# Kernel tuning notes

Hardware: AMD Instinct MI355X
Metric: run time of the kernel (lower is better)

## Reference

```python
import jax, jax.numpy as jnp
import numpy as np

SHIFT_PX = 2
SHIFT_TEMP = 0.07


def _normalize(x):
    # F.normalize(dim=-1): x / max(||x||, eps)
    n = jnp.linalg.norm(x, axis=-1, keepdims=True)
    return x / jnp.maximum(n, 1e-12)


def _weights_to_tokens(w):
    # w: [B,1,H,W] already at target_hw -> bilinear resize is identity
    wf = w.reshape(w.shape[0], -1)
    return wf / (wf.sum(axis=1, keepdims=True) + 1e-10)


def setup_inputs() -> dict:
    key = jax.random.key(0)
    k1, k2, k3, k4 = jax.random.split(key, 4)
    B, H, W, D = 8, 96, 96, 768
    N = H * W
    return {
        "z1": jax.random.normal(k1, (B, N, D), dtype=jnp.float32),
        "z2": jax.random.normal(k2, (B, N, D), dtype=jnp.float32),
        "w1": jax.random.uniform(k3, (B, 1, H, W), dtype=jnp.float32),
        "w2": jax.random.uniform(k4, (B, 1, H, W), dtype=jnp.float32),
        "H": H,
        "W": W,
    }


def reference(z1, z2, w1, w2, H, W):
    B, N, D = z1.shape
    # gs1 == gs2 == target_hw -> token interpolation is the identity shortcut
    z1g = _normalize(z1).reshape(B, H, W, D)
    z2g = _normalize(z2).reshape(B, H, W, D)

    w_avg = 0.5 * (_weights_to_tokens(w1) + _weights_to_tokens(w2))  # [B, N]

    r = SHIFT_PX
    # zero-pad so shifted reads outside the grid contribute zero similarity,
    # matching torch F.pad + slice semantics in the original loop
    z2pad = jnp.pad(z2g, ((0, 0), (r, r), (r, r), (0, 0)))
    sims = []
    for dy in range(-r, r + 1):
        for dx in range(-r, r + 1):
            # z2p[y, x] = z2g[y - dy, x - dx] (zeros out of range)
            z2p = z2pad[:, r - dy:r - dy + H, r - dx:r - dx + W, :]
            sims.append(jnp.einsum('bhwd,bhwd->bhw', z1g, z2p))
    sim_stack = jnp.stack(sims, axis=1)  # [B, (2r+1)^2, H, W]

    alpha = jax.nn.softmax(sim_stack / (SHIFT_TEMP + 1e-10), axis=1)
    sim_softbest = (alpha * sim_stack).sum(axis=1).reshape(B, -1)  # [B, N]

    align_loss = ((1.0 - sim_softbest) * w_avg).sum(axis=1).mean()
    pos_similarity = sim_softbest.mean()
    return jnp.stack([align_loss, pos_similarity])
```

## Files before the change

kernel.cpp:

```cpp
#include <hip/hip_runtime.h>
#include <hip/hip_bf16.h>

#define Bb 8
#define Hh 96
#define Ww 96
#define Dd 768
#define Nn (Hh*Ww)
#define DC 16
#define NCH (Dd/DC)
#define SZ 20
#define TMP 0.07f


__global__ __launch_bounds__(256) void k_wsum(const float* __restrict__ w1,
                                              const float* __restrict__ w2,
                                              float* __restrict__ ws) {
    int j = blockIdx.x;
    const float* src = (j < 8 ? w1 : w2) + (size_t)(j & 7) * Nn;
    float s = 0.f;
    for (int i = threadIdx.x; i < Nn; i += 256) s += src[i];
    for (int off = 32; off > 0; off >>= 1) s += __shfl_down(s, off, 64);
    __shared__ float parts[4];
    int lane = threadIdx.x & 63, wv = threadIdx.x >> 6;
    if (lane == 0) parts[wv] = s;
    __syncthreads();
    if (threadIdx.x == 0) ws[2 + j] = parts[0] + parts[1] + parts[2] + parts[3];
    if (j == 0 && threadIdx.x == 64) ws[0] = 0.f;
    if (j == 0 && threadIdx.x == 65) ws[1] = 0.f;
}

__global__ __launch_bounds__(384, 1) void k_main(
    const float* __restrict__ z1, const float* __restrict__ z2,
    const float* __restrict__ w1, const float* __restrict__ w2,
    float* __restrict__ ws) {
    extern __shared__ float sm[];
    float* z1s  = sm;
    float* z2s  = z1s + 96*SZ;
    float* simS = z2s + 5*100*SZ;
    float* nrm1 = simS + 25*96;
    float* nrm2 = nrm1 + 96;
    float* red  = nrm2 + 480;

    const int t = threadIdx.x;
    const int b = blockIdx.x / Hh;
    const int h = blockIdx.x % Hh;
    const int w = t % 96;
    const int quarter = t / 96;
    const int dq = quarter * 4;

    for (int i = t; i < 5*100*SZ; i += 384) z2s[i] = 0.f;
    for (int i = t; i < 25*96 + 96 + 480 + 2; i += 384) simS[i] = 0.f;

    float acc[5][5] = {};
    float nz2[5]    = {};
    float nz1       = 0.f;

    const size_t zbase = (size_t)b * Nn * Dd;

    for (int c = 0; c < NCH; ++c) {
        const int d0 = c * DC;
        __syncthreads();
        {
            int tok = t >> 2, j = t & 3;
            float4 v = *(const float4*)(z1 + zbase + (size_t)(h*Ww + tok)*Dd + d0 + j*4);
            *(float4*)&z1s[tok*SZ + j*4] = v;
        }
        #pragma unroll
        for (int rep = 0; rep < 5; ++rep) {
            int idx = t + rep*384;
            int rho = idx / 384;
            int rem = idx - rho*384;
            int tok = rem >> 2, j = rem & 3;
            int hr  = h + 2 - rho;
            if (hr >= 0 && hr < Hh) {
                float4 v = *(const float4*)(z2 + zbase + (size_t)(hr*Ww + tok)*Dd + d0 + j*4);
                *(float4*)&z2s[(rho*100 + tok + 2)*SZ + j*4] = v;
            }
        }
        __syncthreads();
        const float4 a = *(const float4*)&z1s[w*SZ + dq];
        nz1 += a.x*a.x + a.y*a.y + a.z*a.z + a.w*a.w;
        #pragma unroll
        for (int rho = 0; rho < 5; ++rho) {
            const float* rowp = &z2s[(rho*100 + w)*SZ + dq];
            #pragma unroll
            for (int k = 0; k < 5; ++k) {
                const float4 q = *(const float4*)(rowp + k*SZ);
                acc[rho][4-k] += a.x*q.x + a.y*q.y + a.z*q.z + a.w*q.w;
                if (k == 2) nz2[rho] += q.x*q.x + q.y*q.y + q.z*q.z + q.w*q.w;
            }
        }
    }

    atomicAdd(&nrm1[w], nz1);
    #pragma unroll
    for (int rho = 0; rho < 5; ++rho) atomicAdd(&nrm2[rho*96 + w], nz2[rho]);
    #pragma unroll
    for (int rho = 0; rho < 5; ++rho)
        #pragma unroll
        for (int del = 0; del < 5; ++del)
            atomicAdd(&simS[(rho*5 + del)*96 + w], acc[rho][del]);
    __syncthreads();

    if (t < 96) {
        const float inv1 = 1.f / fmaxf(sqrtf(nrm1[t]), 1e-12f);
        float sims[25];
        #pragma unroll
        for (int s = 0; s < 25; ++s) {
            int rho = s / 5, del = s % 5;
            int col = t + 2 - del;
            float v = simS[s*96 + t];
            float iv2 = 0.f;
            if (col >= 0 && col < 96) iv2 = 1.f / fmaxf(sqrtf(nrm2[rho*96 + col]), 1e-12f);
            sims[s] = v * inv1 * iv2;
        }
        float m = -1e30f;
        #pragma unroll
        for (int s = 0; s < 25; ++s) m = fmaxf(m, sims[s]);
        float den = 0.f, num = 0.f;
        #pragma unroll
        for (int s = 0; s < 25; ++s) {
            float p = __expf((sims[s] - m) * (1.f / TMP));
            den += p; num += p * sims[s];
        }
        float ssb = num / den;
        int base = b*Nn + h*Ww + t;
        float wa = 0.5f * (w1[base] / (ws[2 + b] + 1e-10f) + w2[base] / (ws[10 + b] + 1e-10f));
        atomicAdd(&red[0], (1.f - ssb) * wa);
        atomicAdd(&red[1], ssb);
    }
    __syncthreads();
    if (t == 0) {
        atomicAdd(&ws[0], red[0]);
        atomicAdd(&ws[1], red[1]);
    }
}

__global__ void k_final(const float* __restrict__ ws, float* __restrict__ out) {
    if (threadIdx.x == 0) {
        out[0] = ws[0] / (float)Bb;
        out[1] = ws[1] / (float)(Bb * Nn);
    }
}

extern "C" void kernel_launch(void* const* d_in, const int* in_sizes, int n_in,
                              void* d_out, int out_size, void* d_ws, size_t ws_size,
                              hipStream_t stream) {
    const float* z1 = (const float*)d_in[0];
    const float* z2 = (const float*)d_in[1];
    const float* w1 = (const float*)d_in[2];
    const float* w2 = (const float*)d_in[3];
    float* ws = (float*)d_ws;
    float* out = (float*)d_out;

    k_wsum<<<16, 256, 0, stream>>>(w1, w2, ws);
    size_t smbytes = (size_t)(96*SZ + 5*100*SZ + 25*96 + 96 + 480 + 2) * sizeof(float);
    k_main<<<Bb*Hh, 384, smbytes, stream>>>(z1, z2, w1, w2, ws);
    k_final<<<1, 64, 0, stream>>>(ws, out);
}
```

Measured before the change: 780.9 us.

## Prefetch next z chunk into registers, shrink LDS, reorder blocks by batch

The main loop now loads the next 16-wide D chunk of z1 and the five z2 rows into registers while computing on the current chunk in LDS, so global loads overlap with compute. The reduction scratch (simS, norms, red) reuses the staging LDS after the loop, which cuts shared memory per block. The launch bound now asks for 5 blocks per CU, which raises occupancy but caps registers per thread. Block indexing is interleaved across batches so blocks running at the same time work on neighbouring rows of different images. The trade-off is more live registers for the prefetch buffers and a tighter register budget.

```diff
diff --git a/kernel.cpp b/kernel.cpp
--- a/kernel.cpp
+++ b/kernel.cpp
@@ -1,5 +1,4 @@
 #include <hip/hip_runtime.h>
-#include <hip/hip_bf16.h>
 
 #define Bb 8
 #define Hh 96
@@ -29,55 +28,61 @@
     if (j == 0 && threadIdx.x == 65) ws[1] = 0.f;
 }
 
-__global__ __launch_bounds__(384, 1) void k_main(
+__global__ __launch_bounds__(384, 5) void k_main(
     const float* __restrict__ z1, const float* __restrict__ z2,
     const float* __restrict__ w1, const float* __restrict__ w2,
     float* __restrict__ ws) {
     extern __shared__ float sm[];
-    float* z1s  = sm;
-    float* z2s  = z1s + 96*SZ;
-    float* simS = z2s + 5*100*SZ;
-    float* nrm1 = simS + 25*96;
-    float* nrm2 = nrm1 + 96;
-    float* red  = nrm2 + 480;
+    float* z1s = sm;
+    float* z2s = sm + 96*SZ;
 
     const int t = threadIdx.x;
-    const int b = blockIdx.x / Hh;
-    const int h = blockIdx.x % Hh;
+    const int b = blockIdx.x & 7;
+    const int h = blockIdx.x >> 3;
     const int w = t % 96;
-    const int quarter = t / 96;
-    const int dq = quarter * 4;
+    const int dq = (t / 96) * 4;
 
     for (int i = t; i < 5*100*SZ; i += 384) z2s[i] = 0.f;
-    for (int i = t; i < 25*96 + 96 + 480 + 2; i += 384) simS[i] = 0.f;
 
     float acc[5][5] = {};
     float nz2[5]    = {};
     float nz1       = 0.f;
 
     const size_t zbase = (size_t)b * Nn * Dd;
+    const int tok = t >> 2, j4 = (t & 3) * 4;
+
+    const float* p1 = z1 + zbase + (size_t)(h*Ww + tok)*Dd + j4;
+    const int wa1 = tok*SZ + j4;
+    const float* p2[5]; bool m2[5]; int wa2[5];
+    #pragma unroll
+    for (int rho = 0; rho < 5; ++rho) {
+        int hr = h + 2 - rho;
+        m2[rho] = (hr >= 0 && hr < Hh);
+        p2[rho] = z2 + zbase + (size_t)((m2[rho] ? hr : 0)*Ww + tok)*Dd + j4;
+        wa2[rho] = (rho*100 + tok + 2)*SZ + j4;
+    }
+
+    float4 r1 = *(const float4*)p1;
+    float4 r2[5];
+    #pragma unroll
+    for (int rho = 0; rho < 5; ++rho)
+        if (m2[rho]) r2[rho] = *(const float4*)p2[rho];
 
     for (int c = 0; c < NCH; ++c) {
-        const int d0 = c * DC;
         __syncthreads();
-        {
-            int tok = t >> 2, j = t & 3;
-            float4 v = *(const float4*)(z1 + zbase + (size_t)(h*Ww + tok)*Dd + d0 + j*4);
-            *(float4*)&z1s[tok*SZ + j*4] = v;
-        }
+        *(float4*)&z1s[wa1] = r1;
         #pragma unroll
-        for (int rep = 0; rep < 5; ++rep) {
-            int idx = t + rep*384;
-            int rho = idx / 384;
-            int rem = idx - rho*384;
-            int tok = rem >> 2, j = rem & 3;
-            int hr  = h + 2 - rho;
-            if (hr >= 0 && hr < Hh) {
-                float4 v = *(const float4*)(z2 + zbase + (size_t)(hr*Ww + tok)*Dd + d0 + j*4);
-                *(float4*)&z2s[(rho*100 + tok + 2)*SZ + j*4] = v;
+        for (int rho = 0; rho < 5; ++rho)
+            if (m2[rho]) *(float4*)&z2s[wa2[rho]] = r2[rho];
+        __syncthreads();
+        if (c + 1 < NCH) {
+            p1 += DC; r1 = *(const float4*)p1;
+            #pragma unroll
+            for (int rho = 0; rho < 5; ++rho) {
+                p2[rho] += DC;
+                if (m2[rho]) r2[rho] = *(const float4*)p2[rho];
             }
         }
-        __syncthreads();
         const float4 a = *(const float4*)&z1s[w*SZ + dq];
         nz1 += a.x*a.x + a.y*a.y + a.z*a.z + a.w*a.w;
         #pragma unroll
@@ -91,6 +96,14 @@
             }
         }
     }
+
+    __syncthreads();
+    float* simS = sm;
+    float* nrm1 = sm + 2400;
+    float* nrm2 = sm + 2496;
+    float* red  = sm + 2976;
+    for (int i = t; i < 2978; i += 384) sm[i] = 0.f;
+    __syncthreads();
 
     atomicAdd(&nrm1[w], nz1);
     #pragma unroll
@@ -154,7 +167,7 @@
     float* out = (float*)d_out;
 
     k_wsum<<<16, 256, 0, stream>>>(w1, w2, ws);
-    size_t smbytes = (size_t)(96*SZ + 5*100*SZ + 25*96 + 96 + 480 + 2) * sizeof(float);
+    size_t smbytes = (size_t)(96*SZ + 5*100*SZ) * sizeof(float);
     k_main<<<Bb*Hh, 384, smbytes, stream>>>(z1, z2, w1, w2, ws);
     k_final<<<1, 64, 0, stream>>>(ws, out);
 }
```

After: 1.056 ms. 35.2% more time.
